# Kernel optimization log

Hardware: AMD Instinct MI355X
Metric: run time of the kernel (lower is better)

Reference implementation:

```python
import jax, jax.numpy as jnp
import numpy as np

N = 50000   # nodes
E = 800000  # edges
R = 8       # relations
B = 4       # bases
NEG = 0.2   # leaky relu slope


def setup_inputs() -> dict:
    key = jax.random.key(0)
    ks = jax.random.split(key, 20)
    s = 0.1
    rn = lambda k, sh: jax.random.normal(k, sh, dtype=jnp.float32) * s
    return {
        "x": jax.random.normal(ks[0], (N, 64), dtype=jnp.float32),
        "edge_index": jax.random.randint(ks[1], (2, E), 0, N),
        "edge_type": jax.random.randint(ks[2], (E,), 0, R),
        # RGCN layer 1 (64 -> 64), basis decomposition
        "basis1": rn(ks[3], (B, 64, 64)), "comp1": rn(ks[4], (R, B)),
        "root1": rn(ks[5], (64, 64)), "brg1": jnp.zeros((64,), jnp.float32),
        # GAT layer 1 (64 -> 32, heads=4, concat -> 128)
        "wg1": rn(ks[6], (64, 128)), "asrc1": rn(ks[7], (4, 32)),
        "adst1": rn(ks[8], (4, 32)), "bg1": jnp.zeros((128,), jnp.float32),
        # RGCN layer 2 (128 -> 32)
        "basis2": rn(ks[9], (B, 128, 32)), "comp2": rn(ks[10], (R, B)),
        "root2": rn(ks[11], (128, 32)), "brg2": jnp.zeros((32,), jnp.float32),
        # GAT layer 2 (32 -> 16, heads=4, concat=False -> mean)
        "wg2": rn(ks[12], (32, 64)), "asrc2": rn(ks[13], (4, 16)),
        "adst2": rn(ks[14], (4, 16)), "bg2": jnp.zeros((16,), jnp.float32),
    }


def rgcn(x, src, dst, etype, basis, comp, root, bias):
    """PyG RGCNConv with basis decomposition, aggr='mean' per relation."""
    n, f = x.shape
    weight = jnp.einsum('rb,bio->rio', comp, basis)          # [R, in, out]
    seg = dst * R + etype                                    # per (node, relation) segment
    msg = x[src]                                             # [E, in] gather
    sums = jax.ops.segment_sum(msg, seg, num_segments=n * R).reshape(n, R, f)
    cnt = jax.ops.segment_sum(jnp.ones((src.shape[0],), x.dtype), seg,
                              num_segments=n * R).reshape(n, R, 1)
    mean = sums / jnp.maximum(cnt, 1.0)                      # [N, R, in]
    return jnp.einsum('nri,rio->no', mean, weight) + x @ root + bias


def gat(x, src, dst, w, a_src, a_dst, bias, heads, out_ch, concat):
    """PyG GATConv: add self loops, edge softmax over incoming edges."""
    n = x.shape[0]
    loop = jnp.arange(n)
    s2 = jnp.concatenate([src, loop])
    d2 = jnp.concatenate([dst, loop])
    h = (x @ w).reshape(n, heads, out_ch)                    # [N, H, C]
    al_src = (h * a_src).sum(-1)                             # [N, H]
    al_dst = (h * a_dst).sum(-1)                             # [N, H]
    e = jax.nn.leaky_relu(al_src[s2] + al_dst[d2], NEG)      # [E2, H]
    m = jax.ops.segment_max(e, d2, num_segments=n)           # stable softmax per dst
    e = jnp.exp(e - m[d2])
    z = jax.ops.segment_sum(e, d2, num_segments=n)
    alpha = e / z[d2]                                        # [E2, H]
    msg = h[s2] * alpha[:, :, None]                          # [E2, H, C]
    out = jax.ops.segment_sum(msg, d2, num_segments=n)       # [N, H, C]
    out = out.reshape(n, heads * out_ch) if concat else out.mean(axis=1)
    return out + bias


def reference(x, edge_index, edge_type,
              basis1, comp1, root1, brg1, wg1, asrc1, adst1, bg1,
              basis2, comp2, root2, brg2, wg2, asrc2, adst2, bg2):
    src, dst = edge_index[0], edge_index[1]
    # i=0: RGCN + relu (dropout p=0)
    x = jax.nn.relu(rgcn(x, src, dst, edge_type, basis1, comp1, root1, brg1))
    # i=1 == 2*pairs-1: GAT concat, NO activation
    x = gat(x, src, dst, wg1, asrc1, adst1, bg1, heads=4, out_ch=32, concat=True)
    # i=2: RGCN + relu
    x = jax.nn.relu(rgcn(x, src, dst, edge_type, basis2, comp2, root2, brg2))
    # i=3: GAT mean-heads + relu
    x = jax.nn.relu(gat(x, src, dst, wg2, asrc2, adst2, bg2, heads=4, out_ch=16, concat=False))
    return jnp.tanh(x)
```

## Files before the change

kernel.cpp:

```cpp
#include <hip/hip_runtime.h>
#include <math.h>

#define NN 50000
#define EE 800000
#define RR 8
#define SLOPE 0.2f
#define SEGS (NN * RR)
#define NTW ((NN + 63) / 64)
#define NBUK 98
#define SEGB 4096
#define EB4 ((EE + 4095) / 4096)

typedef __attribute__((ext_vector_type(8))) short bf16x8;
typedef __attribute__((ext_vector_type(4))) float f32x4;
typedef _Float16 f16;
typedef __attribute__((ext_vector_type(4))) _Float16 h4;
typedef __attribute__((ext_vector_type(8))) _Float16 h8;

__device__ __forceinline__ float leaky(float v) { return v >= 0.f ? v : SLOPE * v; }

__device__ __forceinline__ void fmacc(float4& a, const float4& v, float p) {
    a.x = fmaf(v.x, p, a.x);
    a.y = fmaf(v.y, p, a.y);
    a.z = fmaf(v.z, p, a.z);
    a.w = fmaf(v.w, p, a.w);
}

__device__ __forceinline__ void red4(float4& a, int m) {
    a.x += __shfl_xor(a.x, m);
    a.y += __shfl_xor(a.y, m);
    a.z += __shfl_xor(a.z, m);
    a.w += __shfl_xor(a.w, m);
}

__device__ __forceinline__ float4 h4tof4(h4 t) {
    return make_float4((float)t[0], (float)t[1], (float)t[2], (float)t[3]);
}

__device__ __forceinline__ h4 hmax4(h4 a, h4 b) {
    h4 r;
    r[0] = a[0] > b[0] ? a[0] : b[0];
    r[1] = a[1] > b[1] ? a[1] : b[1];
    r[2] = a[2] > b[2] ? a[2] : b[2];
    r[3] = a[3] > b[3] ? a[3] : b[3];
    return r;
}

__device__ __forceinline__ void split8(const float4& v0, const float4& v1,
                                       bf16x8& hi, bf16x8& lo) {
    float e[8] = {v0.x, v0.y, v0.z, v0.w, v1.x, v1.y, v1.z, v1.w};
    union { bf16x8 v; unsigned u[4]; } H, L;
#pragma unroll
    for (int j = 0; j < 4; j++) {
        unsigned b0 = __float_as_uint(e[2 * j]), b1 = __float_as_uint(e[2 * j + 1]);
        unsigned h0 = b0 & 0xFFFF0000u, h1 = b1 & 0xFFFF0000u;
        H.u[j] = (h0 >> 16) | h1;
        float l0 = e[2 * j] - __uint_as_float(h0);
        float l1 = e[2 * j + 1] - __uint_as_float(h1);
        L.u[j] = (__float_as_uint(l0) >> 16) | (__float_as_uint(l1) & 0xFFFF0000u);
    }
    hi = H.v;
    lo = L.v;
}

__global__ __launch_bounds__(256) void k_hist(const int* __restrict__ dst,
                                              int* __restrict__ buccnt) {
    __shared__ int h[NBUK];
    int tid = threadIdx.x;
    for (int i = tid; i < NBUK; i += 256) h[i] = 0;
    __syncthreads();
    int e0 = blockIdx.x * 4096;
    int cnt = EE - e0;
    if (cnt > 4096) cnt = 4096;
    for (int i = tid; i < cnt; i += 256) atomicAdd(&h[dst[e0 + i] >> 9], 1);
    __syncthreads();
    for (int i = tid; i < NBUK; i += 256)
        if (h[i]) atomicAdd(&buccnt[i], h[i]);
}

__global__ void k_scan98(const int* __restrict__ buccnt, int* __restrict__ bucbase,
                         int* __restrict__ cbcur) {
    __shared__ int sh[128];
    int t = threadIdx.x;
    int v = (t < NBUK) ? buccnt[t] : 0;
    sh[t] = v;
    __syncthreads();
    for (int off = 1; off < 128; off <<= 1) {
        int u = (t >= off) ? sh[t - off] : 0;
        __syncthreads();
        sh[t] += u;
        __syncthreads();
    }
    int excl = sh[t] - v;
    if (t <= NBUK) bucbase[t] = excl;
    if (t < NBUK) cbcur[t] = excl;
}

__global__ __launch_bounds__(256) void k_fillA(const int* __restrict__ src,
                                               const int* __restrict__ dst,
                                               const int* __restrict__ et,
                                               int* __restrict__ cbcur,
                                               int* __restrict__ recbuf) {
    __shared__ int hist[NBUK], lcur[NBUK], gres[NBUK];
    int tid = threadIdx.x;
    int e0 = blockIdx.x * 4096;
    int cnt = EE - e0;
    if (cnt > 4096) cnt = 4096;
    for (int i = tid; i < NBUK; i += 256) { hist[i] = 0; lcur[i] = 0; }
    __syncthreads();
    int myb[16], myrec[16];
#pragma unroll
    for (int j = 0; j < 16; j++) {
        int i = tid + j * 256;
        if (i < cnt) {
            int e = e0 + i;
            int d = dst[e];
            int b = d >> 9;
            myb[j] = b;
            myrec[j] = ((d & 511) << 19) | (src[e] << 3) | et[e];
            atomicAdd(&hist[b], 1);
        } else {
            myb[j] = -1;
            myrec[j] = 0;
        }
    }
    __syncthreads();
    if (tid < NBUK) gres[tid] = atomicAdd(&cbcur[tid], hist[tid]);
    __syncthreads();
#pragma unroll
    for (int j = 0; j < 16; j++) {
        if (myb[j] >= 0) {
            int p = atomicAdd(&lcur[myb[j]], 1);
            recbuf[gres[myb[j]] + p] = myrec[j];
        }
    }
}

__global__ __launch_bounds__(256) void k_fillB2(const int* __restrict__ bucbase,
                                                const int* __restrict__ recbuf,
                                                int* __restrict__ rp,
                                                int* __restrict__ srcs2) {
    __shared__ int cnt[SEGB];
    __shared__ int psc[256];
    int b = blockIdx.x;
    int segbase = b * SEGB;
    int nseg = SEGS - segbase;
    if (nseg > SEGB) nseg = SEGB;
    int base = bucbase[b];
    int cntE = bucbase[b + 1] - base;
    int tid = threadIdx.x;
    for (int s = tid; s < SEGB; s += 256) cnt[s] = 0;
    __syncthreads();
    for (int i = tid; i < cntE; i += 256) {
        int rec = recbuf[base + i];
        int segl = ((rec >> 19) << 3) | (rec & 7);
        atomicAdd(&cnt[segl], 1);
    }
    __syncthreads();
    int loc[16];
    int sbase = tid * 16;
    int run = 0;
#pragma unroll
    for (int j = 0; j < 16; j++) { loc[j] = cnt[sbase + j]; run += loc[j]; }
    psc[tid] = run;
    __syncthreads();
    for (int off = 1; off < 256; off <<= 1) {
        int u = (tid >= off) ? psc[tid - off] : 0;
        __syncthreads();
        psc[tid] += u;
        __syncthreads();
    }
    int excl = psc[tid] - run;
#pragma unroll
    for (int j = 0; j < 16; j++) {
        int s = sbase + j;
        int v = loc[j];
        cnt[s] = excl;
        if (s < nseg) rp[segbase + s] = base + excl;
        excl += v;
    }
    __syncthreads();
    for (int i = tid; i < cntE; i += 256) {
        int rec = recbuf[base + i];
        int segl = ((rec >> 19) << 3) | (rec & 7);
        int p = atomicAdd(&cnt[segl], 1);
        srcs2[base + p] = rec & 0x7FFFF;
    }
    if (b == NBUK - 1 && tid == 0) rp[SEGS] = EE;
}

__global__ void k_xh(const float* __restrict__ X, f16* __restrict__ xh) {
    int i = blockIdx.x * 256 + threadIdx.x;
    if (i >= NN * 8) return;
    float4 v0 = *(const float4*)(X + (size_t)i * 8);
    float4 v1 = *(const float4*)(X + (size_t)i * 8 + 4);
    h8 hv = {(f16)v0.x, (f16)v0.y, (f16)v0.z, (f16)v0.w,
             (f16)v1.x, (f16)v1.y, (f16)v1.z, (f16)v1.w};
    *(h8*)(xh + (size_t)i * 8) = hv;
}

__global__ void k_prep(const float* __restrict__ wg1, const float* __restrict__ wg2,
                       const float* __restrict__ root1, const float* __restrict__ root2,
                       const float* __restrict__ basis1, const float* __restrict__ basis2,
                       const float* __restrict__ comp2,
                       const float* __restrict__ asrc1, const float* __restrict__ adst1,
                       const float* __restrict__ asrc2, const float* __restrict__ adst2,
                       float* __restrict__ Wcat2e, float* __restrict__ wg1r,
                       float* __restrict__ Wstk, float* __restrict__ U1p,
                       float* __restrict__ U2p, float* __restrict__ Wb1) {
    int idx = blockIdx.x * 256 + threadIdx.x;
    if (idx < 16384) {
        int h = idx >> 12, kc = idx & 4095;
        int k = kc >> 6, c = kc & 63;
        wg1r[idx] = (c < 32) ? wg1[k * 128 + h * 32 + c] : 0.f;
    } else if (idx < 24576) {
        int j = idx - 16384;
        int row = j >> 6, c = j & 63;
        int h = row >> 5, k = row & 31;
        Wstk[j] = (c < 16) ? wg2[k * 64 + h * 16 + c] : 0.f;
    } else if (idx < 32768) {
        int j = idx - 24576;
        int k = j >> 6, c = j & 63;
        Wcat2e[k * 320 + c] = (c < 32) ? root2[k * 32 + c] : 0.f;
    } else if (idx < 36864) {
        int j0 = idx - 32768;
        int k = j0 >> 6, j = j0 & 63;
        float s = 0.f;
        if (j < 8) {
            int h = j & 3;
            const float* a = (j < 4) ? asrc1 : adst1;
            for (int c = 0; c < 32; c++) s += wg1[k * 128 + h * 32 + c] * a[h * 32 + c];
        }
        U1p[j0] = s;
    } else if (idx < 38912) {
        int j0 = idx - 36864;
        int k = j0 >> 6, j = j0 & 63;
        float s = 0.f;
        if (j < 8) {
            int h = j & 3;
            const float* a = (j < 4) ? asrc2 : adst2;
            for (int c = 0; c < 16; c++) s += wg2[k * 64 + h * 16 + c] * a[h * 16 + c];
        }
        U2p[j0] = s;
    } else if (idx < 55296) {
        Wb1[idx - 38912] = basis1[idx - 38912];
    } else if (idx < 59392) {
        Wb1[idx - 38912] = root1[idx - 55296];
    } else if (idx < 92160) {
        int j = idx - 59392;
        int i = j >> 8, rc = j & 255;
        int r = rc >> 5, o = rc & 31;
        float acc = 0.f;
#pragma unroll
        for (int b = 0; b < 4; b++) acc += comp2[r * 4 + b] * basis2[b * 4096 + i * 32 + o];
        Wcat2e[i * 320 + 64 + rc] = acc;
    }
}

__global__ void k_pack(const float* __restrict__ Wb1, const float* __restrict__ wg1r,
                       const float* __restrict__ Wcat, short* __restrict__ pWb1,
                       short* __restrict__ pwg1r, short* __restrict__ pWcat) {
    int u = blockIdx.x * 256 + threadIdx.x;
    int lane = u & 63, pair = u >> 6;
    if (pair >= 136) return;
    int m = lane & 15, g = lane >> 4;
    const float* src;
    int ldB, col, k0;
    short* dst;
    if (pair < 40) {
        int ct = pair / 10, kc = pair % 10;
        src = Wb1; ldB = 64; col = ct * 16 + m; k0 = kc * 32 + g * 8;
        dst = pWb1 + pair * 1024 + lane * 8;
    } else if (pair < 56) {
        int q = pair - 40;
        int h = q >> 2, lp = q & 3, ct = lp >> 1, kc = lp & 1;
        src = wg1r + h * 4096; ldB = 64; col = ct * 16 + m; k0 = kc * 32 + g * 8;
        dst = pwg1r + q * 1024 + lane * 8;
    } else {
        int q = pair - 56;
        int p = q >> 4, lp = q & 15, ct = lp >> 2, kc = lp & 3;
        src = Wcat; ldB = 320; col = p * 64 + ct * 16 + m; k0 = kc * 32 + g * 8;
        dst = pWcat + q * 1024 + lane * 8;
    }
    float e[8];
#pragma unroll
    for (int r = 0; r < 8; r++) e[r] = src[(size_t)(k0 + r) * ldB + col];
    union { bf16x8 v; unsigned u4[4]; } H, L;
#pragma unroll
    for (int j = 0; j < 4; j++) {
        unsigned b0 = __float_as_uint(e[2 * j]), b1 = __float_as_uint(e[2 * j + 1]);
        unsigned h0 = b0 & 0xFFFF0000u, h1 = b1 & 0xFFFF0000u;
        H.u4[j] = (h0 >> 16) | h1;
        float l0 = e[2 * j] - __uint_as_float(h0);
        float l1 = e[2 * j + 1] - __uint_as_float(h1);
        L.u4[j] = (__float_as_uint(l0) >> 16) | (__float_as_uint(l1) & 0xFFFF0000u);
    }
    *(bf16x8*)dst = H.v;
    *(bf16x8*)(dst + 512) = L.v;
}

template <int KTOT, int NCOL, int ACT = 0, int OUTH = 0, int AH = 0>
__global__ __launch_bounds__(256) void k_mfma(const float* __restrict__ X, int ldX, int xmb,
                                              const short* __restrict__ Bpk, int bmb,
                                              float* __restrict__ Y, int ldY, size_t ymb,
                                              const float* __restrict__ bias, int biasmb) {
    constexpr int NKC = KTOT / 32;
    constexpr int NCT = NCOL / 16;
    const int tid = threadIdx.x;
    const int wid = tid >> 6, lane = tid & 63;
    const int m = lane & 15, g = lane >> 4;
    const int mb = blockIdx.y;
    const int rowbase = blockIdx.x * 64 + wid * 16;
    if (rowbase >= NN) return;
    const float* Xm = X + (size_t)mb * xmb + (size_t)(rowbase + m) * ldX;
    const f16* Xmh = (const f16*)X + (size_t)mb * xmb + (size_t)(rowbase + m) * ldX;
    const short* Bm = Bpk + (size_t)mb * bmb;

    f32x4 acc[NCT];
#pragma unroll
    for (int c = 0; c < NCT; c++) acc[c] = (f32x4){0.f, 0.f, 0.f, 0.f};

#pragma unroll
    for (int kc = 0; kc < NKC; kc++) {
        float4 v0, v1;
        if (AH) {
            h8 hv = *(const h8*)(Xmh + kc * 32 + g * 8);
            v0 = make_float4((float)hv[0], (float)hv[1], (float)hv[2], (float)hv[3]);
            v1 = make_float4((float)hv[4], (float)hv[5], (float)hv[6], (float)hv[7]);
        } else {
            v0 = *(const float4*)(Xm + kc * 32 + g * 8);
            v1 = *(const float4*)(Xm + kc * 32 + g * 8 + 4);
        }
        bf16x8 ah, al;
        split8(v0, v1, ah, al);
#pragma unroll
        for (int ct = 0; ct < NCT; ct++) {
            const short* bp = Bm + (size_t)(ct * NKC + kc) * 1024 + lane * 8;
            bf16x8 bh = *(const bf16x8*)bp;
            bf16x8 bl = *(const bf16x8*)(bp + 512);
            acc[ct] = __builtin_amdgcn_mfma_f32_16x16x32_bf16(ah, bh, acc[ct], 0, 0, 0);
            acc[ct] = __builtin_amdgcn_mfma_f32_16x16x32_bf16(al, bh, acc[ct], 0, 0, 0);
            acc[ct] = __builtin_amdgcn_mfma_f32_16x16x32_bf16(ah, bl, acc[ct], 0, 0, 0);
        }
    }

#pragma unroll
    for (int ct = 0; ct < NCT; ct++) {
        int col = ct * 16 + m;
        float bv = bias ? bias[mb * biasmb + col] : 0.f;
#pragma unroll
        for (int i = 0; i < 4; i++) {
            float o = acc[ct][i] + bv;
            if (ACT == 2) o = fmaxf(o, 0.f);
            if (OUTH) {
                f16* Yh = (f16*)Y;
                Yh[(size_t)mb * ymb + (size_t)(rowbase + g * 4 + i) * ldY + col] = (f16)o;
            } else {
                Y[(size_t)mb * ymb + (size_t)(rowbase + g * 4 + i) * ldY + col] = o;
            }
        }
    }
}

__global__ __launch_bounds__(256) void k_gagg1(const int* __restrict__ rp,
                                               const int* __restrict__ srcs2,
                                               const float* __restrict__ comp,
                                               const f16* __restrict__ Xh,
                                               f16* __restrict__ Uh) {
    __shared__ float4 sh_w[4][8];
    int wid = threadIdx.x >> 6, lane = threadIdx.x & 63;
    int n = blockIdx.x * 4 + wid;
    int rpv = (lane <= 8) ? rp[n * RR + lane] : 0;
    int nxt = __shfl(rpv, (lane + 1) & 63);
    if (lane < 8) {
        float inv = 1.f / (float)((nxt - rpv) > 0 ? (nxt - rpv) : 1);
        float4 c = *(const float4*)(comp + lane * 4);
        sh_w[wid][lane] = make_float4(c.x * inv, c.y * inv, c.z * inv, c.w * inv);
    }
    int q = lane & 15;
    int beg = rp[n * RR], end = rp[n * RR + RR];
    float4 a0 = make_float4(0.f, 0.f, 0.f, 0.f);
    float4 a1 = a0, a2 = a0, a3 = a0;
    int k = beg + (lane >> 4);
    for (; k + 4 < end; k += 8) {
        int key0 = srcs2[k], key1 = srcs2[k + 4];
        float4 w0 = sh_w[wid][key0 & 7], w1 = sh_w[wid][key1 & 7];
        float4 v0 = h4tof4(*(const h4*)(Xh + (size_t)(key0 >> 3) * 64 + q * 4));
        float4 v1 = h4tof4(*(const h4*)(Xh + (size_t)(key1 >> 3) * 64 + q * 4));
        fmacc(a0, v0, w0.x);
        fmacc(a1, v0, w0.y);
        fmacc(a2, v0, w0.z);
        fmacc(a3, v0, w0.w);
        fmacc(a0, v1, w1.x);
        fmacc(a1, v1, w1.y);
        fmacc(a2, v1, w1.z);
        fmacc(a3, v1, w1.w);
    }
    if (k < end) {
        int key0 = srcs2[k];
        float4 w0 = sh_w[wid][key0 & 7];
        float4 v0 = h4tof4(*(const h4*)(Xh + (size_t)(key0 >> 3) * 64 + q * 4));
        fmacc(a0, v0, w0.x);
        fmacc(a1, v0, w0.y);
        fmacc(a2, v0, w0.z);
        fmacc(a3, v0, w0.w);
    }
    red4(a0, 16); red4(a0, 32);
    red4(a1, 16); red4(a1, 32);
    red4(a2, 16); red4(a2, 32);
    red4(a3, 16); red4(a3, 32);
    if (lane < 16) {
        f16* un = Uh + (size_t)n * 320;
        h4 o0 = {(f16)a0.x, (f16)a0.y, (f16)a0.z, (f16)a0.w};
        h4 o1 = {(f16)a1.x, (f16)a1.y, (f16)a1.z, (f16)a1.w};
        h4 o2 = {(f16)a2.x, (f16)a2.y, (f16)a2.z, (f16)a2.w};
        h4 o3 = {(f16)a3.x, (f16)a3.y, (f16)a3.z, (f16)a3.w};
        *(h4*)(un + 0 * 64 + q * 4) = o0;
        *(h4*)(un + 1 * 64 + q * 4) = o1;
        *(h4*)(un + 2 * 64 + q * 4) = o2;
        *(h4*)(un + 3 * 64 + q * 4) = o3;
        *(h4*)(un + 256 + q * 4) = *(const h4*)(Xh + (size_t)n * 64 + q * 4);
    }
}

__global__ __launch_bounds__(256) void k_alds1(const float* __restrict__ X,
                                               const float* __restrict__ U1p,
                                               f16* __restrict__ aldsEh,
                                               f16* __restrict__ x1h) {
    __shared__ float sUT[8 * 68];
    int tid = threadIdx.x;
    for (int i = tid; i < 512; i += 256) {
        int j = i >> 6, c = i & 63;
        sUT[j * 68 + c] = U1p[c * 64 + j];
    }
    __syncthreads();
    int lane = tid & 63, wid = tid >> 6;
    int n = blockIdx.x * 32 + wid * 8 + (lane >> 3);
    int q = lane & 7;
    float x[8];
    if (n < NN) {
        float4 v0 = *(const float4*)(X + (size_t)n * 64 + q * 8);
        float4 v1 = *(const float4*)(X + (size_t)n * 64 + q * 8 + 4);
        x[0] = v0.x; x[1] = v0.y; x[2] = v0.z; x[3] = v0.w;
        x[4] = v1.x; x[5] = v1.y; x[6] = v1.z; x[7] = v1.w;
        h8 hv;
#pragma unroll
        for (int c = 0; c < 8; c++) hv[c] = (f16)x[c];
        *(h8*)(x1h + (size_t)n * 64 + q * 8) = hv;
    } else {
#pragma unroll
        for (int c = 0; c < 8; c++) x[c] = 0.f;
    }
    float al[8];
#pragma unroll
    for (int j = 0; j < 8; j++) {
        const float* u = &sUT[j * 68 + q * 8];
        float s = 0.f;
#pragma unroll
        for (int c = 0; c < 8; c++) s += x[c] * u[c];
        al[j] = s;
    }
#pragma unroll
    for (int m = 1; m < 8; m <<= 1)
#pragma unroll
        for (int j = 0; j < 8; j++) al[j] += __shfl_xor(al[j], m);
    if (n < NN) {
        float av = al[q];
        int pos = (q < 4) ? q : q + 4;
        aldsEh[(size_t)n * 16 + pos] = (f16)__expf(av);
        aldsEh[(size_t)n * 16 + pos + 4] = (f16)__expf(SLOPE * av);
    }
}

__global__ __launch_bounds__(256) void k_final(const f16* __restrict__ Xm,
                                               const float* __restrict__ Wstk,
                                               const float* __restrict__ bg2,
                                               float* __restrict__ out) {
    __shared__ float sWT[16 * 132];
    int tid = threadIdx.x;
    for (int i = tid; i < 2048; i += 256) {
        int c = i >> 7, k = i & 127;
        sWT[c * 132 + k] = Wstk[k * 64 + c];
    }
    __syncthreads();
    int lane = tid & 63, wid = tid >> 6;
    int n = blockIdx.x * 32 + wid * 8 + (lane >> 3);
    int q = lane & 7;
    float x[16];
    if (n < NN) {
#pragma unroll
        for (int t = 0; t < 4; t++) {
            float4 v = h4tof4(*(const h4*)(Xm + (size_t)n * 128 + t * 32 + q * 4));
            x[t * 4 + 0] = v.x; x[t * 4 + 1] = v.y; x[t * 4 + 2] = v.z; x[t * 4 + 3] = v.w;
        }
    } else {
#pragma unroll
        for (int k = 0; k < 16; k++) x[k] = 0.f;
    }
    float al[16];
#pragma unroll
    for (int c = 0; c < 16; c++) {
        float s = 0.f;
#pragma unroll
        for (int t = 0; t < 4; t++) {
            const float* w = &sWT[c * 132 + t * 32 + q * 4];
            s += x[t * 4 + 0] * w[0] + x[t * 4 + 1] * w[1] + x[t * 4 + 2] * w[2] +
                 x[t * 4 + 3] * w[3];
        }
        al[c] = s;
    }
#pragma unroll
    for (int m = 1; m < 8; m <<= 1)
#pragma unroll
        for (int c = 0; c < 16; c++) al[c] += __shfl_xor(al[c], m);
    if (n < NN && q < 4) {
        float4 bv = *(const float4*)(bg2 + q * 4);
        float4 v;
        v.x = tanhf(fmaxf(0.25f * al[q * 4 + 0] + bv.x, 0.f));
        v.y = tanhf(fmaxf(0.25f * al[q * 4 + 1] + bv.y, 0.f));
        v.z = tanhf(fmaxf(0.25f * al[q * 4 + 2] + bv.z, 0.f));
        v.w = tanhf(fmaxf(0.25f * al[q * 4 + 3] + bv.w, 0.f));
        *(float4*)(out + (size_t)n * 16 + q * 4) = v;
    }
}

__global__ __launch_bounds__(256) void k_agg2(const int* __restrict__ rp,
                                              const int* __restrict__ srcs2,
                                              const f16* __restrict__ y,
                                              const float* __restrict__ bias,
                                              const float* __restrict__ U2p,
                                              const float* __restrict__ x3prev,
                                              f16* __restrict__ x3h,
                                              f16* __restrict__ aldsEh) {
    __shared__ float sh_inv[4][8];
    int wid = threadIdx.x >> 6, lane = threadIdx.x & 63;
    int n = blockIdx.x * 4 + wid;
    int rpv = (lane <= 8) ? rp[n * RR + lane] : 0;
    int nxt = __shfl(rpv, (lane + 1) & 63);
    if (lane < 8) sh_inv[wid][lane] = 1.f / (float)((nxt - rpv) > 0 ? (nxt - rpv) : 1);
    int q = lane & 7;
    int beg = rp[n * RR], end = rp[n * RR + RR];
    float4 acc = make_float4(0.f, 0.f, 0.f, 0.f);
    int k = beg + (lane >> 3);
    for (; k + 8 < end; k += 16) {
        int key0 = srcs2[k], key1 = srcs2[k + 8];
        int s0 = key0 >> 3, s1 = key1 >> 3;
        int g0 = key0 & 7, g1 = key1 & 7;
        float e0 = sh_inv[wid][g0], e1 = sh_inv[wid][g1];
        float4 v0 = h4tof4(*(const h4*)(y + ((size_t)(g0 >> 1) * NN + s0) * 64 + (g0 & 1) * 32 + q * 4));
        float4 v1 = h4tof4(*(const h4*)(y + ((size_t)(g1 >> 1) * NN + s1) * 64 + (g1 & 1) * 32 + q * 4));
        fmacc(acc, v0, e0);
        fmacc(acc, v1, e1);
    }
    if (k < end) {
        int key0 = srcs2[k];
        int s0 = key0 >> 3;
        int g0 = key0 & 7;
        float4 v0 = h4tof4(*(const h4*)(y + ((size_t)(g0 >> 1) * NN + s0) * 64 + (g0 & 1) * 32 + q * 4));
        fmacc(acc, v0, sh_inv[wid][g0]);
    }
    red4(acc, 8);
    red4(acc, 16);
    red4(acc, 32);
    if (lane < 8) {
        float4 prev = *(const float4*)(x3prev + (size_t)n * 64 + q * 4);
        float4 b = *(const float4*)(bias + q * 4);
        float4 v;
        v.x = fmaxf(prev.x + acc.x + b.x, 0.f);
        v.y = fmaxf(prev.y + acc.y + b.y, 0.f);
        v.z = fmaxf(prev.z + acc.z + b.z, 0.f);
        v.w = fmaxf(prev.w + acc.w + b.w, 0.f);
        h4 hv = {(f16)v.x, (f16)v.y, (f16)v.z, (f16)v.w};
        *(h4*)(x3h + (size_t)n * 32 + q * 4) = hv;
        float al[8];
#pragma unroll
        for (int j = 0; j < 8; j++) {
            al[j] = fmaf(v.x, U2p[(q * 4 + 0) * 64 + j],
                    fmaf(v.y, U2p[(q * 4 + 1) * 64 + j],
                    fmaf(v.z, U2p[(q * 4 + 2) * 64 + j],
                         v.w * U2p[(q * 4 + 3) * 64 + j])));
        }
#pragma unroll
        for (int m = 1; m < 8; m <<= 1) {
#pragma unroll
            for (int j = 0; j < 8; j++) al[j] += __shfl_xor(al[j], m);
        }
        float av = al[q];
        int pos = (q < 4) ? q : q + 4;
        aldsEh[(size_t)n * 16 + pos] = (f16)__expf(av);
        aldsEh[(size_t)n * 16 + pos + 4] = (f16)__expf(SLOPE * av);
    }
}

template <int F, int LDX = F>
__global__ __launch_bounds__(256) void k_gatx(const int* __restrict__ rp,
                                              const int* __restrict__ srcs2,
                                              const f16* __restrict__ aldsEh,
                                              const f16* __restrict__ X,
                                              f16* __restrict__ msg) {
    constexpr int G = F / 4;
    constexpr int NG = 64 / G;
    int wid = threadIdx.x >> 6, lane = threadIdx.x & 63;
    int n = blockIdx.x * 4 + wid;
    if (n >= NN) return;
    int g = lane / G, q = lane % G;
    h4 EdH = *(const h4*)(aldsEh + (size_t)n * 16 + 8);
    h4 Ed2H = *(const h4*)(aldsEh + (size_t)n * 16 + 12);
    float4 acc0 = make_float4(0.f, 0.f, 0.f, 0.f);
    float4 acc1 = acc0, acc2 = acc0, acc3 = acc0;
    float4 z = make_float4(0.f, 0.f, 0.f, 0.f);
    if (g == 0) {
        h4 es = *(const h4*)(aldsEh + (size_t)n * 16);
        h4 es2 = *(const h4*)(aldsEh + (size_t)n * 16 + 4);
        float4 xv = h4tof4(*(const h4*)(X + (size_t)n * LDX + q * 4));
        h4 pH = hmax4(es * EdH, es2 * Ed2H);
        float p0 = (float)pH[0], p1 = (float)pH[1], p2 = (float)pH[2], p3 = (float)pH[3];
        z = make_float4(p0, p1, p2, p3);
        fmacc(acc0, xv, p0);
        fmacc(acc1, xv, p1);
        fmacc(acc2, xv, p2);
        fmacc(acc3, xv, p3);
    }
    int beg = rp[n * RR], end = rp[n * RR + RR];
    int k = beg + g;
    for (; k + NG < end; k += 2 * NG) {
        int s0 = srcs2[k] >> 3, s1 = srcs2[k + NG] >> 3;
        h8 e0 = *(const h8*)(aldsEh + (size_t)s0 * 16);
        h8 e1 = *(const h8*)(aldsEh + (size_t)s1 * 16);
        float4 x0 = h4tof4(*(const h4*)(X + (size_t)s0 * LDX + q * 4));
        float4 x1v = h4tof4(*(const h4*)(X + (size_t)s1 * LDX + q * 4));
        h4 e0lo = {e0[0], e0[1], e0[2], e0[3]};
        h4 e0hi = {e0[4], e0[5], e0[6], e0[7]};
        h4 e1lo = {e1[0], e1[1], e1[2], e1[3]};
        h4 e1hi = {e1[4], e1[5], e1[6], e1[7]};
        h4 p0H = hmax4(e0lo * EdH, e0hi * Ed2H);
        h4 p1H = hmax4(e1lo * EdH, e1hi * Ed2H);
        float p00 = (float)p0H[0], p01 = (float)p0H[1], p02 = (float)p0H[2], p03 = (float)p0H[3];
        float p10 = (float)p1H[0], p11 = (float)p1H[1], p12 = (float)p1H[2], p13 = (float)p1H[3];
        z.x += p00 + p10;
        z.y += p01 + p11;
        z.z += p02 + p12;
        z.w += p03 + p13;
        fmacc(acc0, x0, p00);
        fmacc(acc1, x0, p01);
        fmacc(acc2, x0, p02);
        fmacc(acc3, x0, p03);
        fmacc(acc0, x1v, p10);
        fmacc(acc1, x1v, p11);
        fmacc(acc2, x1v, p12);
        fmacc(acc3, x1v, p13);
    }
    if (k < end) {
        int s0 = srcs2[k] >> 3;
        h8 e0 = *(const h8*)(aldsEh + (size_t)s0 * 16);
        float4 x0 = h4tof4(*(const h4*)(X + (size_t)s0 * LDX + q * 4));
        h4 e0lo = {e0[0], e0[1], e0[2], e0[3]};
        h4 e0hi = {e0[4], e0[5], e0[6], e0[7]};
        h4 p0H = hmax4(e0lo * EdH, e0hi * Ed2H);
        float p00 = (float)p0H[0], p01 = (float)p0H[1], p02 = (float)p0H[2], p03 = (float)p0H[3];
        z.x += p00;
        z.y += p01;
        z.z += p02;
        z.w += p03;
        fmacc(acc0, x0, p00);
        fmacc(acc1, x0, p01);
        fmacc(acc2, x0, p02);
        fmacc(acc3, x0, p03);
    }
#pragma unroll
    for (int m = G; m < 64; m <<= 1) {
        red4(acc0, m);
        red4(acc1, m);
        red4(acc2, m);
        red4(acc3, m);
        red4(z, m);
    }
    if (g == 0) {
        float4 iz = make_float4(1.f / z.x, 1.f / z.y, 1.f / z.z, 1.f / z.w);
        f16* mp = msg + (size_t)n * 4 * F + q * 4;
        h4 o0 = {(f16)(acc0.x * iz.x), (f16)(acc0.y * iz.x), (f16)(acc0.z * iz.x), (f16)(acc0.w * iz.x)};
        h4 o1 = {(f16)(acc1.x * iz.y), (f16)(acc1.y * iz.y), (f16)(acc1.z * iz.y), (f16)(acc1.w * iz.y)};
        h4 o2 = {(f16)(acc2.x * iz.z), (f16)(acc2.y * iz.z), (f16)(acc2.z * iz.z), (f16)(acc2.w * iz.z)};
        h4 o3 = {(f16)(acc3.x * iz.w), (f16)(acc3.y * iz.w), (f16)(acc3.z * iz.w), (f16)(acc3.w * iz.w)};
        *(h4*)(mp + 0 * F) = o0;
        *(h4*)(mp + 1 * F) = o1;
        *(h4*)(mp + 2 * F) = o2;
        *(h4*)(mp + 3 * F) = o3;
    }
}

extern "C" void kernel_launch(void* const* d_in, const int* in_sizes, int n_in,
                              void* d_out, int out_size, void* d_ws, size_t ws_size,
                              hipStream_t stream) {
    const float* x      = (const float*)d_in[0];
    const int*   ei     = (const int*)d_in[1];
    const int*   et     = (const int*)d_in[2];
    const float* basis1 = (const float*)d_in[3];
    const float* comp1  = (const float*)d_in[4];
    const float* root1  = (const float*)d_in[5];
    const float* brg1   = (const float*)d_in[6];
    const float* wg1    = (const float*)d_in[7];
    const float* asrc1  = (const float*)d_in[8];
    const float* adst1  = (const float*)d_in[9];
    const float* bg1    = (const float*)d_in[10];
    const float* basis2 = (const float*)d_in[11];
    const float* comp2  = (const float*)d_in[12];
    const float* root2  = (const float*)d_in[13];
    const float* brg2   = (const float*)d_in[14];
    const float* wg2    = (const float*)d_in[15];
    const float* asrc2  = (const float*)d_in[16];
    const float* adst2  = (const float*)d_in[17];
    const float* bg2    = (const float*)d_in[18];
    const int* src = ei;
    const int* dst = ei + EE;
    float* out = (float*)d_out;

    int* wsi = (int*)d_ws;
    size_t ioff = 0;
    auto ialloc = [&](size_t n) { int* p = wsi + ioff; ioff += (n + 3) & ~(size_t)3; return p; };
    int* rp   = ialloc(SEGS + 1);
    int* srcs2 = ialloc(EE);
    int* recbuf = ialloc(EE);
    int* cbcur = ialloc(128);
    int* buccnt = ialloc(128);
    int* bucbase = ialloc(128);
    float* wsf = (float*)(wsi + ioff);
    size_t total_f = (ws_size - ioff * sizeof(int)) / sizeof(float);
    size_t P_f = (size_t)NN * 320;
    size_t need_f = P_f + (size_t)NN * 128
                  + 40960 + 20480 + 16384 + 8192 + 4096 + 2048
                  + (size_t)NN * 8
                  + 20480 + 8192 + 40960
                  + (size_t)NN * 32 + (size_t)NN * 16 + (size_t)NN * 32 + 64;
    if (total_f < need_f) return;
    size_t foff = 0;
    auto falloc = [&](size_t n) { float* p = wsf + foff; foff += (n + 3) & ~(size_t)3; return p; };
    float* P      = falloc(P_f);
    float* x2     = falloc((size_t)NN * 128);
    float* Wcat2e = falloc(40960);
    float* Wb1    = falloc(20480);
    float* wg1r   = falloc(16384);
    float* Wstk   = falloc(8192);
    float* U1p    = falloc(4096);
    float* U2p    = falloc(2048);
    f16* aldsEh   = (f16*)falloc((size_t)NN * 8);
    short* Wb1pk  = (short*)falloc(20480);
    short* wg1rpk = (short*)falloc(8192);
    short* Wcatpk = (short*)falloc(40960);
    f16* x1h      = (f16*)falloc((size_t)NN * 32);
    f16* x3h      = (f16*)falloc((size_t)NN * 16);
    f16* xh       = (f16*)falloc((size_t)NN * 32);
    f16* Uh = (f16*)P;
    float* x1   = x2 + (size_t)NN * 64;
    f16* msg1h  = (f16*)P;
    float* x3   = P;
    f16* ybuf3h = (f16*)(P + (size_t)NN * 64);
    f16* msg2h  = (f16*)(P + (size_t)NN * 64);

    const int NB4 = (NN + 3) / 4;
    const int NB32 = (NN + 31) / 32;

    hipMemsetAsync(buccnt, 0, 128 * sizeof(int), stream);
    k_hist<<<EB4, 256, 0, stream>>>(dst, buccnt);
    k_scan98<<<1, 128, 0, stream>>>(buccnt, bucbase, cbcur);
    k_fillA<<<EB4, 256, 0, stream>>>(src, dst, et, cbcur, recbuf);
    k_fillB2<<<NBUK, 256, 0, stream>>>(bucbase, recbuf, rp, srcs2);
    k_xh<<<(NN * 8 + 255) / 256, 256, 0, stream>>>(x, xh);
    k_prep<<<(92160 + 255) / 256, 256, 0, stream>>>(
        wg1, wg2, root1, root2, basis1, basis2, comp2, asrc1, adst1, asrc2, adst2,
        Wcat2e, wg1r, Wstk, U1p, U2p, Wb1);
    k_pack<<<34, 256, 0, stream>>>(Wb1, wg1r, Wcat2e, Wb1pk, wg1rpk, Wcatpk);

    k_gagg1<<<NB4, 256, 0, stream>>>(rp, srcs2, comp1, xh, Uh);
    k_mfma<320, 64, 2, 0, 1><<<dim3(NTW, 1), 256, 0, stream>>>((const float*)Uh, 320, 0,
                                                               Wb1pk, 0,
                                                               x1, 64, 0, brg1, 0);

    k_alds1<<<NB32, 256, 0, stream>>>(x1, U1p, aldsEh, x1h);
    k_gatx<64, 64><<<NB4, 256, 0, stream>>>(rp, srcs2, aldsEh, x1h, msg1h);
    k_mfma<64, 32, 0, 0, 1><<<dim3(NTW, 4), 256, 0, stream>>>((const float*)msg1h, 256, 64,
                                                              wg1rpk, 4096,
                                                              x2, 128, 32, bg1, 32);

    k_mfma<128, 64, 0, 0><<<dim3(NTW, 1), 256, 0, stream>>>(x2, 128, 0, Wcatpk, 0,
                                                            P, 64, 0, nullptr, 0);
    k_mfma<128, 64, 0, 1><<<dim3(NTW, 4), 256, 0, stream>>>(x2, 128, 0, Wcatpk + 16384, 16384,
                                                            (float*)ybuf3h, 64, (size_t)NN * 64,
                                                            nullptr, 0);
    k_agg2<<<NB4, 256, 0, stream>>>(rp, srcs2, ybuf3h, brg2, U2p, x3, x3h, aldsEh);

    k_gatx<32, 32><<<NB4, 256, 0, stream>>>(rp, srcs2, aldsEh, x3h, msg2h);
    k_final<<<NB32, 256, 0, stream>>>(msg2h, Wstk, bg2, out);
}
```

Baseline: 403.1 us.

## Store layer intermediates in fp16 and fuse layer-2 RGCN GEMMs into one kernel

The first RGCN GEMM and the GAT-1 projection GEMM now write fp16 outputs directly, so k_alds1 no longer converts x1 to fp16 and reads half the bytes. The two separate layer-2 GEMMs (root/self part and the per-basis projections) are replaced by one k_mfmaL3 kernel that reads x2 once as fp16 and computes all 18 column tiles. The root part is stored compactly with 32 columns per row instead of 64. This reduces memory traffic and launches, at the cost of 18 accumulator tiles per wave, which raises register pressure, and of fp16 rounding of x2, though the GEMM still uses split-bf16 for accuracy.

```diff
diff --git a/kernel.cpp b/kernel.cpp
--- a/kernel.cpp
+++ b/kernel.cpp
@@ -362,6 +362,61 @@
     }
 }
 
+__global__ __launch_bounds__(256) void k_mfmaL3(const f16* __restrict__ Xh,
+                                                const short* __restrict__ Bpk,
+                                                float* __restrict__ x3,
+                                                f16* __restrict__ ybuf3h) {
+    const int tid = threadIdx.x;
+    const int wid = tid >> 6, lane = tid & 63;
+    const int m = lane & 15, g = lane >> 4;
+    const int rowbase = blockIdx.x * 64 + wid * 16;
+    if (rowbase >= NN) return;
+    const f16* Xm = Xh + (size_t)(rowbase + m) * 128;
+
+    f32x4 acc[18];
+#pragma unroll
+    for (int i = 0; i < 18; i++) acc[i] = (f32x4){0.f, 0.f, 0.f, 0.f};
+
+#pragma unroll
+    for (int kc = 0; kc < 4; kc++) {
+        h8 hv = *(const h8*)(Xm + kc * 32 + g * 8);
+        float4 v0 = make_float4((float)hv[0], (float)hv[1], (float)hv[2], (float)hv[3]);
+        float4 v1 = make_float4((float)hv[4], (float)hv[5], (float)hv[6], (float)hv[7]);
+        bf16x8 ah, al;
+        split8(v0, v1, ah, al);
+#pragma unroll
+        for (int i = 0; i < 18; i++) {
+            int bct = (i < 2) ? i : i + 2;
+            const short* bp = Bpk + (size_t)(bct * 4 + kc) * 1024 + lane * 8;
+            bf16x8 bh = *(const bf16x8*)bp;
+            bf16x8 bl = *(const bf16x8*)(bp + 512);
+            acc[i] = __builtin_amdgcn_mfma_f32_16x16x32_bf16(ah, bh, acc[i], 0, 0, 0);
+            acc[i] = __builtin_amdgcn_mfma_f32_16x16x32_bf16(al, bh, acc[i], 0, 0, 0);
+            acc[i] = __builtin_amdgcn_mfma_f32_16x16x32_bf16(ah, bl, acc[i], 0, 0, 0);
+        }
+    }
+#pragma unroll
+    for (int i = 0; i < 2; i++) {
+        int col = i * 16 + m;
+#pragma unroll
+        for (int r = 0; r < 4; r++) {
+            int n = rowbase + g * 4 + r;
+            x3[(size_t)n * 32 + col] = acc[i][r];
+        }
+    }
+#pragma unroll
+    for (int i = 2; i < 18; i++) {
+        int gcol = (i + 2) * 16 + m - 64;
+        int p = gcol >> 6, cc = gcol & 63;
+        f16* Yp = ybuf3h + (size_t)p * NN * 64;
+#pragma unroll
+        for (int r = 0; r < 4; r++) {
+            int n = rowbase + g * 4 + r;
+            Yp[(size_t)n * 64 + cc] = (f16)acc[i][r];
+        }
+    }
+}
+
 __global__ __launch_bounds__(256) void k_gagg1(const int* __restrict__ rp,
                                                const int* __restrict__ srcs2,
                                                const float* __restrict__ comp,
@@ -423,10 +478,9 @@
     }
 }
 
-__global__ __launch_bounds__(256) void k_alds1(const float* __restrict__ X,
+__global__ __launch_bounds__(256) void k_alds1(const f16* __restrict__ X1h,
                                                const float* __restrict__ U1p,
-                                               f16* __restrict__ aldsEh,
-                                               f16* __restrict__ x1h) {
+                                               f16* __restrict__ aldsEh) {
     __shared__ float sUT[8 * 68];
     int tid = threadIdx.x;
     for (int i = tid; i < 512; i += 256) {
@@ -439,14 +493,9 @@
     int q = lane & 7;
     float x[8];
     if (n < NN) {
-        float4 v0 = *(const float4*)(X + (size_t)n * 64 + q * 8);
-        float4 v1 = *(const float4*)(X + (size_t)n * 64 + q * 8 + 4);
-        x[0] = v0.x; x[1] = v0.y; x[2] = v0.z; x[3] = v0.w;
-        x[4] = v1.x; x[5] = v1.y; x[6] = v1.z; x[7] = v1.w;
-        h8 hv;
-#pragma unroll
-        for (int c = 0; c < 8; c++) hv[c] = (f16)x[c];
-        *(h8*)(x1h + (size_t)n * 64 + q * 8) = hv;
+        h8 hv = *(const h8*)(X1h + (size_t)n * 64 + q * 8);
+#pragma unroll
+        for (int c = 0; c < 8; c++) x[c] = (float)hv[c];
     } else {
 #pragma unroll
         for (int c = 0; c < 8; c++) x[c] = 0.f;
@@ -563,7 +612,7 @@
     red4(acc, 16);
     red4(acc, 32);
     if (lane < 8) {
-        float4 prev = *(const float4*)(x3prev + (size_t)n * 64 + q * 4);
+        float4 prev = *(const float4*)(x3prev + (size_t)n * 32 + q * 4);
         float4 b = *(const float4*)(bias + q * 4);
         float4 v;
         v.x = fmaxf(prev.x + acc.x + b.x, 0.f);
@@ -751,7 +800,7 @@
     f16* x3h      = (f16*)falloc((size_t)NN * 16);
     f16* xh       = (f16*)falloc((size_t)NN * 32);
     f16* Uh = (f16*)P;
-    float* x1   = x2 + (size_t)NN * 64;
+    f16* x2h = (f16*)x2;
     f16* msg1h  = (f16*)P;
     float* x3   = P;
     f16* ybuf3h = (f16*)(P + (size_t)NN * 64);
@@ -772,21 +821,17 @@
     k_pack<<<34, 256, 0, stream>>>(Wb1, wg1r, Wcat2e, Wb1pk, wg1rpk, Wcatpk);
 
     k_gagg1<<<NB4, 256, 0, stream>>>(rp, srcs2, comp1, xh, Uh);
-    k_mfma<320, 64, 2, 0, 1><<<dim3(NTW, 1), 256, 0, stream>>>((const float*)Uh, 320, 0,
+    k_mfma<320, 64, 2, 1, 1><<<dim3(NTW, 1), 256, 0, stream>>>((const float*)Uh, 320, 0,
                                                                Wb1pk, 0,
-                                                               x1, 64, 0, brg1, 0);
-
-    k_alds1<<<NB32, 256, 0, stream>>>(x1, U1p, aldsEh, x1h);
+                                                               (float*)x1h, 64, 0, brg1, 0);
+
+    k_alds1<<<NB32, 256, 0, stream>>>(x1h, U1p, aldsEh);
     k_gatx<64, 64><<<NB4, 256, 0, stream>>>(rp, srcs2, aldsEh, x1h, msg1h);
-    k_mfma<64, 32, 0, 0, 1><<<dim3(NTW, 4), 256, 0, stream>>>((const float*)msg1h, 256, 64,
+    k_mfma<64, 32, 0, 1, 1><<<dim3(NTW, 4), 256, 0, stream>>>((const float*)msg1h, 256, 64,
                                                               wg1rpk, 4096,
-                                                              x2, 128, 32, bg1, 32);
-
-    k_mfma<128, 64, 0, 0><<<dim3(NTW, 1), 256, 0, stream>>>(x2, 128, 0, Wcatpk, 0,
-                                                            P, 64, 0, nullptr, 0);
-    k_mfma<128, 64, 0, 1><<<dim3(NTW, 4), 256, 0, stream>>>(x2, 128, 0, Wcatpk + 16384, 16384,
-                                                            (float*)ybuf3h, 64, (size_t)NN * 64,
-                                                            nullptr, 0);
+                                                              (float*)x2h, 128, 32, bg1, 32);
+
+    k_mfmaL3<<<NTW, 256, 0, stream>>>(x2h, Wcatpk, x3, ybuf3h);
     k_agg2<<<NB4, 256, 0, stream>>>(rp, srcs2, ybuf3h, brg2, U2p, x3, x3h, aldsEh);
 
     k_gatx<32, 32><<<NB4, 256, 0, stream>>>(rp, srcs2, aldsEh, x3h, msg2h);
```

Result: faster. 395.0 us (-2.0%).
